# Kernel tuning notes

Measured on AMD Instinct MI355X. Metric: run time of the kernel, lower is better.

## Reference

```python
import jax, jax.numpy as jnp
import numpy as np

N_EMBD = 1024
HEAD_SIZE = 128
B, T = 8, 4096


def setup_inputs() -> dict:
    key = jax.random.key(0)
    ks = jax.random.split(key, 7)
    s = 1.0 / np.sqrt(N_EMBD)
    return {
        "x": jax.random.normal(ks[0], (B, T, N_EMBD), dtype=jnp.float32),
        "Wq": jax.random.uniform(ks[1], (N_EMBD, HEAD_SIZE), jnp.float32, -s, s),
        "bq": jax.random.uniform(ks[2], (HEAD_SIZE,), jnp.float32, -s, s),
        "Wk": jax.random.uniform(ks[3], (N_EMBD, HEAD_SIZE), jnp.float32, -s, s),
        "bk": jax.random.uniform(ks[4], (HEAD_SIZE,), jnp.float32, -s, s),
        "Wv": jax.random.uniform(ks[5], (N_EMBD, HEAD_SIZE), jnp.float32, -s, s),
        "bv": jax.random.uniform(ks[6], (HEAD_SIZE,), jnp.float32, -s, s),
    }


def reference(x, Wq, bq, Wk, bk, Wv, bv):
    # q,k,v: [B,T,H]
    q = x @ Wq + bq
    k = x @ Wk + bk
    v = x @ Wv + bv
    scale = HEAD_SIZE ** -0.5
    att = jnp.einsum("bth,bsh->bts", q, k) * scale  # [B,T,T]
    t = x.shape[1]
    causal = jnp.tril(jnp.ones((t, t), dtype=bool))
    att = jnp.where(causal, att, -jnp.inf)
    att = jax.nn.softmax(att, axis=-1)
    # dropout with p=0.0 is identity (eval-mode equivalent)
    out = jnp.einsum("bts,bsh->bth", att, v)  # [B,T,H]
    return out
```

## Files before the change

kernel.cpp:

```cpp
#include <hip/hip_runtime.h>
#include <hip/hip_bf16.h>
#include <stdint.h>

#define BATCH 8
#define SEQ   4096
#define EMB   1024
#define HD    128
#define NROWS 32768

typedef __attribute__((ext_vector_type(8))) short short8;
typedef __attribute__((ext_vector_type(4))) float f32x4;

__device__ inline unsigned short f2bf(float f) {
    union { float f; unsigned int u; } c; c.f = f;
    unsigned int u = c.u;
    unsigned int r = (u + 0x7fffu + ((u >> 16) & 1u)) >> 16;
    return (unsigned short)r;
}
__device__ inline float bf2f(unsigned short u) {
    union { unsigned int i; float f; } c; c.i = ((unsigned int)u) << 16; return c.f;
}
__device__ inline unsigned int pkbf(float a, float b) {
    __hip_bfloat162 h = __float22bfloat162_rn(make_float2(a, b));
    union { __hip_bfloat162 h; unsigned int u; } c; c.h = h; return c.u;
}

#define GLDS16(gp, lp) __builtin_amdgcn_global_load_lds( \
    (const __attribute__((address_space(1))) void*)(gp), \
    (__attribute__((address_space(3))) void*)(lp), 16, 0, 0)

__device__ inline void decomp(int it, int& b, int& qt, int& kv) {
    b = it / 2112;
    int r = it - b * 2112;
    int q = (int)((__builtin_sqrtf(2.0f * (float)r + 1.0f) - 1.0f) * 0.5f);
    while (2 * (q + 1) * (q + 2) <= r) ++q;
    while (2 * q * (q + 1) > r) --q;
    qt = q;
    kv = r - 2 * q * (q + 1);
}
__device__ inline int base1(int qt) {
    if (qt < 5)  return qt;
    if (qt < 11) return 5 + 2 * (qt - 5);
    if (qt < 16) return 17 + 3 * (qt - 11);
    if (qt < 22) return 32 + 4 * (qt - 16);
    if (qt < 27) return 56 + 5 * (qt - 22);
    return 81 + 6 * (qt - 27);
}

__global__ __launch_bounds__(256) void prep_kernel(
    const float* __restrict__ Wq, const float* __restrict__ bq,
    const float* __restrict__ Wk, const float* __restrict__ bk,
    const float* __restrict__ Wv, const float* __restrict__ bv,
    unsigned short* __restrict__ wt, float* __restrict__ biasc)
{
    const int n = blockIdx.x;
    const int sel = n >> 7, h = n & 127;
    const float* W = (sel == 0) ? Wq : (sel == 1) ? Wk : Wv;
    const int tid = threadIdx.x;
    const int k0 = tid * 4;
    union { unsigned short us[4]; uint2 v; } pk;
#pragma unroll
    for (int u = 0; u < 4; ++u) pk.us[u] = f2bf(W[(size_t)(k0 + u) * HD + h]);
    *(uint2*)&wt[(size_t)n * EMB + k0] = pk.v;
    if (tid == 0) {
        const float* bp = (sel == 0) ? bq : (sel == 1) ? bk : bv;
        biasc[n] = bp[h];
    }
}

__global__ __launch_bounds__(768, 3) void gemm_qkv(
    const float* __restrict__ x, const unsigned short* __restrict__ wt,
    const float* __restrict__ biasc,
    unsigned short* __restrict__ q, unsigned short* __restrict__ kOut,
    unsigned short* __restrict__ vt)
{
    const int m0  = blockIdx.x * 128;
    const int tid = threadIdx.x;
    const int wave = tid >> 6, lane = tid & 63;
    const int quad = lane >> 4, l15 = lane & 15;
    const int wm = (wave >= 6) ? 1 : 0;
    const int wn = wave - wm * 6;

    __shared__ __align__(16) unsigned short As[2][128][40];
    __shared__ __align__(16) unsigned short Bs[2][12288];

    f32x4 acc[4][4];
#pragma unroll
    for (int i = 0; i < 4; ++i)
#pragma unroll
        for (int j = 0; j < 4; ++j) acc[i][j] = (f32x4){0.f, 0.f, 0.f, 0.f};

    const int aactive = (tid < 512);
    const int arow = tid >> 3, akc = (tid & 7) * 4;
    float4 aR0, aR1;

#define LOAD_A(kt)                                                          \
    if (aactive) {                                                          \
        aR0 = *(const float4*)(x + (size_t)(m0 + arow) * EMB + (kt) * 32 + akc);        \
        aR1 = *(const float4*)(x + (size_t)(m0 + arow + 64) * EMB + (kt) * 32 + akc);   \
    }
#define WRITE_A(buf)                                                        \
    if (aactive) {                                                          \
        union { unsigned short us[4]; uint2 v; } p0, p1;                    \
        p0.us[0] = f2bf(aR0.x); p0.us[1] = f2bf(aR0.y);                     \
        p0.us[2] = f2bf(aR0.z); p0.us[3] = f2bf(aR0.w);                     \
        *(uint2*)&As[buf][arow][akc] = p0.v;                                \
        p1.us[0] = f2bf(aR1.x); p1.us[1] = f2bf(aR1.y);                     \
        p1.us[2] = f2bf(aR1.z); p1.us[3] = f2bf(aR1.w);                     \
        *(uint2*)&As[buf][arow + 64][akc] = p1.v;                           \
    }
#define STAGE_B(kt, buf)                                                    \
    {                                                                       \
        _Pragma("unroll")                                                   \
        for (int g = 0; g < 2; ++g) {                                       \
            int s0 = (g * 12 + wave) * 64;                                  \
            int s  = s0 + lane;                                             \
            int n  = s >> 2, c = (s & 3) ^ (n & 3);                         \
            GLDS16(wt + (size_t)n * EMB + (kt) * 32 + c * 8,                \
                   &Bs[buf][s0 * 8]);                                       \
        }                                                                   \
    }

    LOAD_A(0); STAGE_B(0, 0); WRITE_A(0);
    int cur = 0;

    for (int kt = 0; kt < 32; ++kt) {
        __syncthreads();
        if (kt < 31) { LOAD_A(kt + 1); STAGE_B(kt + 1, cur ^ 1); }
        short8 af[4], bw[4];
#pragma unroll
        for (int mj = 0; mj < 4; ++mj)
            af[mj] = *(const short8*)&As[cur][wm * 64 + mj * 16 + l15][quad * 8];
#pragma unroll
        for (int ni = 0; ni < 4; ++ni) {
            int n = wn * 64 + ni * 16 + l15;
            bw[ni] = *(const short8*)&Bs[cur][n * 32 + ((quad ^ (n & 3)) << 3)];
        }
#pragma unroll
        for (int ni = 0; ni < 4; ++ni)
#pragma unroll
            for (int mj = 0; mj < 4; ++mj)
                acc[ni][mj] = __builtin_amdgcn_mfma_f32_16x16x32_bf16(
                    bw[ni], af[mj], acc[ni][mj], 0, 0, 0);
        if (kt < 31) WRITE_A(cur ^ 1);
        cur ^= 1;
    }

    const float qscale = 0.08838834764831845f * 1.4426950408889634f;
    const int bb = m0 >> 12;
    const int t0 = m0 & 4095;
    const int mrow0 = m0 + wm * 64;
    const int tl0   = t0 + wm * 64;
#pragma unroll
    for (int ni = 0; ni < 4; ++ni) {
        int colbase = wn * 64 + ni * 16;
        int sel = colbase >> 7;
        int c0 = colbase + quad * 4;
        float4 bv4 = *(const float4*)&biasc[c0];
#pragma unroll
        for (int mj = 0; mj < 4; ++mj) {
            int m = mrow0 + mj * 16 + l15;
            if (sel == 0) {
                union { unsigned short us[4]; uint2 v; } pk;
#pragma unroll
                for (int j = 0; j < 4; ++j)
                    pk.us[j] = f2bf((acc[ni][mj][j] + ((const float*)&bv4)[j]) * qscale);
                *(uint2*)&q[(size_t)m * HD + (c0 & 127)] = pk.v;
            } else if (sel == 1) {
                union { unsigned short us[4]; uint2 v; } pk;
#pragma unroll
                for (int j = 0; j < 4; ++j)
                    pk.us[j] = f2bf(acc[ni][mj][j] + ((const float*)&bv4)[j]);
                *(uint2*)&kOut[(size_t)m * HD + (c0 & 127)] = pk.v;
            } else {
#pragma unroll
                for (int j = 0; j < 4; ++j) {
                    int h = (c0 & 127) + j;
                    vt[((size_t)(bb * 128 + h)) * SEQ + tl0 + mj * 16 + l15] =
                        f2bf(acc[ni][mj][j] + ((const float*)&bv4)[j]);
                }
            }
        }
    }
#undef LOAD_A
#undef WRITE_A
#undef STAGE_B
}

__global__ __launch_bounds__(256, 3) void attn_kernel(
    const unsigned short* __restrict__ q, const unsigned short* __restrict__ k,
    const unsigned short* __restrict__ vt, float* __restrict__ out,
    float* __restrict__ Oseg, float2* __restrict__ ml)
{
    const int rank  = blockIdx.x;
    const int chunk = (rank & 7) * 96 + (rank >> 3);
    const int start = chunk * 22;
    const int iend  = start + 22;

    const int tid  = threadIdx.x;
    const int wave = tid >> 6, lane = tid & 63;
    const int quad = lane >> 4, l15 = lane & 15;

    __shared__ __align__(16) unsigned short Ks[2][4096];
    __shared__ __align__(16) unsigned short Vs[2][4096];

    const int bpa0 = (l15 + 16 * ((2 * quad) & 3)) * 4;
    const int bpa1 = (l15 + 16 * ((2 * quad + 1) & 3)) * 4;

#define STAGE_KV(b_, kv_, buf_)                                              \
    {                                                                        \
        const size_t kb0 = (size_t)(b_) * SEQ + (kv_) * 32;                  \
        const size_t vb0 = (size_t)(b_) * HD * SEQ + (kv_) * 32;             \
        _Pragma("unroll")                                                    \
        for (int g = 0; g < 2; ++g) {                                        \
            int s0 = (g * 4 + wave) * 64;                                    \
            int s  = s0 + lane;                                              \
            int key = s >> 4, c = (s & 15) ^ (key & 15);                     \
            GLDS16(k + (kb0 + key) * HD + c * 8, &Ks[buf_][s0 * 8]);         \
        }                                                                    \
        _Pragma("unroll")                                                    \
        for (int g = 0; g < 2; ++g) {                                        \
            int s0 = (g * 4 + wave) * 64;                                    \
            int s  = s0 + lane;                                              \
            int h = s >> 2, c = (s & 3) ^ ((h >> 2) & 3);                    \
            GLDS16(vt + vb0 + (size_t)h * SEQ + c * 8, &Vs[buf_][s0 * 8]);   \
        }                                                                    \
    }

    int b, qt, kv;
    decomp(start, b, qt, kv);

    short8 qf[2][4];
    f32x4  o[2][8];
    float  m_r[2], l_r[2];
    int    qrow0 = 0;

#define CTX_INIT(b_, q_)                                                     \
    {                                                                        \
        qrow0 = (q_) * 128 + wave * 32;                                      \
        const size_t qoff = (size_t)(b_) * SEQ + qrow0;                      \
        _Pragma("unroll")                                                    \
        for (int mi = 0; mi < 2; ++mi)                                       \
            _Pragma("unroll")                                                \
            for (int kh = 0; kh < 4; ++kh)                                   \
                qf[mi][kh] = *(const short8*)(q + (qoff + mi * 16 + l15) * HD + kh * 32 + quad * 8); \
        _Pragma("unroll")                                                    \
        for (int mi = 0; mi < 2; ++mi) {                                     \
            _Pragma("unroll")                                                \
            for (int hi = 0; hi < 8; ++hi) o[mi][hi] = (f32x4){0.f, 0.f, 0.f, 0.f}; \
            m_r[mi] = -1e30f; l_r[mi] = 0.f;                                 \
        }                                                                    \
    }

#define CTX_FLUSH()                                                          \
    {                                                                        \
        const int I0 = b * 2112 + 2 * qt * (qt + 1);                         \
        const int j  = chunk - I0 / 22;                                      \
        const int rr = wave * 32;                                            \
        float* obase;                                                        \
        if (j == 0) obase = out + ((size_t)b * SEQ + qrow0) * HD;            \
        else obase = Oseg + ((size_t)(b * 112 + base1(qt) + j - 1) * 128 + rr) * HD; \
        const size_t mlb = ((size_t)(b * 32 + qt) * 7 + j) * 128 + rr;       \
        _Pragma("unroll")                                                    \
        for (int mi = 0; mi < 2; ++mi) {                                     \
            if (quad == 0) ml[mlb + mi * 16 + l15] = make_float2(m_r[mi], l_r[mi]); \
            _Pragma("unroll")                                                \
            for (int hi = 0; hi < 8; ++hi)                                   \
                *(f32x4*)&obase[(size_t)(mi * 16 + l15) * HD + hi * 16 + quad * 4] = o[mi][hi]; \
        }                                                                    \
    }

#define SMAX(sarr, mi_, pk_)                                                 \
    {                                                                        \
        float mx = fmaxf(fmaxf(fmaxf(sarr[0][0], sarr[0][1]),               \
                               fmaxf(sarr[0][2], sarr[0][3])),              \
                         fmaxf(fmaxf(sarr[1][0], sarr[1][1]),               \
                               fmaxf(sarr[1][2], sarr[1][3])));             \
        mx = fmaxf(mx, __shfl_xor(mx, 16));                                  \
        mx = fmaxf(mx, __shfl_xor(mx, 32));                                  \
        if (!__all(mx - m_r[mi_] <= 8.0f)) {                                 \
            float mnew = fmaxf(m_r[mi_], mx);                                \
            float alpha = __builtin_amdgcn_exp2f(m_r[mi_] - mnew);           \
            m_r[mi_] = mnew;                                                 \
            l_r[mi_] *= alpha;                                               \
            _Pragma("unroll")                                                \
            for (int hi = 0; hi < 8; ++hi) o[mi_][hi] *= alpha;              \
        }                                                                    \
        const float mcur = m_r[mi_];                                         \
        float rs = 0.f;                                                      \
        _Pragma("unroll")                                                    \
        for (int ni = 0; ni < 2; ++ni) {                                     \
            float p0 = __builtin_amdgcn_exp2f(sarr[ni][0] - mcur);           \
            float p1 = __builtin_amdgcn_exp2f(sarr[ni][1] - mcur);           \
            float p2 = __builtin_amdgcn_exp2f(sarr[ni][2] - mcur);           \
            float p3 = __builtin_amdgcn_exp2f(sarr[ni][3] - mcur);           \
            rs += (p0 + p1) + (p2 + p3);                                     \
            pk_[ni][0] = pkbf(p0, p1);                                       \
            pk_[ni][1] = pkbf(p2, p3);                                       \
        }                                                                    \
        rs += __shfl_xor(rs, 16);                                            \
        rs += __shfl_xor(rs, 32);                                            \
        l_r[mi_] += rs;                                                      \
    }

#define BPERM(pk_, pT_)                                                      \
    {                                                                        \
        union { unsigned int u[4]; short8 s8; } pt;                          \
        unsigned int a0 = (unsigned)__builtin_amdgcn_ds_bpermute(bpa0, (int)pk_[0][0]); \
        unsigned int b0 = (unsigned)__builtin_amdgcn_ds_bpermute(bpa0, (int)pk_[1][0]); \
        pt.u[0] = (quad < 2) ? a0 : b0;                                      \
        unsigned int a1 = (unsigned)__builtin_amdgcn_ds_bpermute(bpa0, (int)pk_[0][1]); \
        unsigned int b1 = (unsigned)__builtin_amdgcn_ds_bpermute(bpa0, (int)pk_[1][1]); \
        pt.u[1] = (quad < 2) ? a1 : b1;                                      \
        unsigned int a2 = (unsigned)__builtin_amdgcn_ds_bpermute(bpa1, (int)pk_[0][0]); \
        unsigned int b2 = (unsigned)__builtin_amdgcn_ds_bpermute(bpa1, (int)pk_[1][0]); \
        pt.u[2] = (quad < 2) ? a2 : b2;                                      \
        unsigned int a3 = (unsigned)__builtin_amdgcn_ds_bpermute(bpa1, (int)pk_[0][1]); \
        unsigned int b3 = (unsigned)__builtin_amdgcn_ds_bpermute(bpa1, (int)pk_[1][1]); \
        pt.u[3] = (quad < 2) ? a3 : b3;                                      \
        pT_ = pt.s8;                                                         \
    }

    STAGE_KV(b, kv, 0);
    CTX_INIT(b, qt);
    int cur = 0;

    for (int it = start; it < iend; ++it) {
        const bool more = (it + 1 < iend);
        int b2 = b, qt2 = qt, kv2 = kv + 1;
        const bool ctxend = (kv2 == 4 * qt + 4);
        if (ctxend) { kv2 = 0; ++qt2; if (qt2 == 32) { qt2 = 0; ++b2; } }

        __syncthreads();
        if (more) STAGE_KV(b2, kv2, cur ^ 1);

        const int key0 = kv * 32;
        if (key0 <= qrow0 + 31) {
            f32x4 s0[2], s1[2];
#pragma unroll
            for (int ni = 0; ni < 2; ++ni) { s0[ni] = (f32x4){0.f,0.f,0.f,0.f}; s1[ni] = (f32x4){0.f,0.f,0.f,0.f}; }
            __builtin_amdgcn_s_setprio(1);
#pragma unroll
            for (int kh = 0; kh < 4; ++kh) {
#pragma unroll
                for (int ni = 0; ni < 2; ++ni) {
                    short8 kf = *(const short8*)&Ks[cur][(ni * 16 + l15) * 128 + (((kh * 4 + quad) ^ l15) << 3)];
                    s0[ni] = __builtin_amdgcn_mfma_f32_16x16x32_bf16(kf, qf[0][kh], s0[ni], 0, 0, 0);
                    s1[ni] = __builtin_amdgcn_mfma_f32_16x16x32_bf16(kf, qf[1][kh], s1[ni], 0, 0, 0);
                }
            }
            __builtin_amdgcn_s_setprio(0);
            if (key0 + 31 > qrow0) {
#pragma unroll
                for (int ni = 0; ni < 2; ++ni)
#pragma unroll
                    for (int j = 0; j < 4; ++j) {
                        int key = key0 + ni * 16 + quad * 4 + j;
                        if (key > qrow0 + l15)      s0[ni][j] = -1e30f;
                        if (key > qrow0 + 16 + l15) s1[ni][j] = -1e30f;
                    }
            }
            unsigned int pk0[2][2], pk1[2][2];
            short8 pT0, pT1;
            SMAX(s0, 0, pk0)
            BPERM(pk0, pT0)
            SMAX(s1, 1, pk1)
            BPERM(pk1, pT1)
            __builtin_amdgcn_s_setprio(1);
#pragma unroll
            for (int hi = 0; hi < 8; ++hi) {
                short8 vf = *(const short8*)&Vs[cur][(hi * 16 + l15) * 32 + ((quad ^ (l15 >> 2)) << 3)];
                o[0][hi] = __builtin_amdgcn_mfma_f32_16x16x32_bf16(vf, pT0, o[0][hi], 0, 0, 0);
                o[1][hi] = __builtin_amdgcn_mfma_f32_16x16x32_bf16(vf, pT1, o[1][hi], 0, 0, 0);
            }
            __builtin_amdgcn_s_setprio(0);
        }

        if (ctxend || !more) {
            CTX_FLUSH();
            if (more && ctxend) CTX_INIT(b2, qt2);
        }
        b = b2; qt = qt2; kv = kv2;
        cur ^= 1;
    }
#undef STAGE_KV
#undef CTX_INIT
#undef CTX_FLUSH
#undef SMAX
#undef BPERM
}

__global__ __launch_bounds__(256) void merge_kernel(
    float* __restrict__ out, const float* __restrict__ Oseg,
    const float2* __restrict__ ml)
{
    int idx = blockIdx.x * 256 + threadIdx.x;
    int row = idx >> 5;
    int hc  = (idx & 31) << 2;
    int b = row >> 12, t = row & 4095, qt = t >> 7, rr = t & 127;
    int I0   = b * 2112 + 2 * qt * (qt + 1);
    int n    = 4 * (qt + 1);
    int nseg = (I0 + n - 1) / 22 - I0 / 22 + 1;

    const float2* mlp = ml + ((size_t)(b * 32 + qt) * 7) * 128 + rr;
    float2 s0 = mlp[0];
    float M = s0.x;
    for (int j = 1; j < nseg; ++j) M = fmaxf(M, mlp[(size_t)j * 128].x);

    float w0 = __builtin_amdgcn_exp2f(s0.x - M);
    float L  = w0 * s0.y;
    f32x4 a = *(const f32x4*)&out[(size_t)row * HD + hc];
    a = a * w0;
    for (int j = 1; j < nseg; ++j) {
        float2 mj = mlp[(size_t)j * 128];
        float w = __builtin_amdgcn_exp2f(mj.x - M);
        L += w * mj.y;
        const float* sp = Oseg + ((size_t)(b * 112 + base1(qt) + j - 1) * 128 + rr) * HD + hc;
        f32x4 sv = *(const f32x4*)sp;
        a = a + sv * w;
    }
    float inv = 1.0f / L;
    *(f32x4*)&out[(size_t)row * HD + hc] = a * inv;
}

extern "C" void kernel_launch(void* const* d_in, const int* in_sizes, int n_in,
                              void* d_out, int out_size, void* d_ws, size_t ws_size,
                              hipStream_t stream) {
    const float* x  = (const float*)d_in[0];
    const float* Wq = (const float*)d_in[1];
    const float* bq = (const float*)d_in[2];
    const float* Wk = (const float*)d_in[3];
    const float* bk = (const float*)d_in[4];
    const float* Wv = (const float*)d_in[5];
    const float* bv = (const float*)d_in[6];
    float* out = (float*)d_out;

    unsigned short* wt    = (unsigned short*)d_ws;
    float*          biasc = (float*)((char*)d_ws + 786432);
    unsigned short* qb    = (unsigned short*)((char*)d_ws + 787968);
    unsigned short* kb    = qb  + (size_t)NROWS * HD;
    unsigned short* vtb   = kb  + (size_t)NROWS * HD;
    float*          Oseg  = (float*)((char*)d_ws + 787968 + 3ull * NROWS * HD * 2);
    float2*         mlseg = (float2*)((char*)Oseg + 896ull * 128 * HD * 4);

    prep_kernel<<<dim3(384), 256, 0, stream>>>(Wq, bq, Wk, bk, Wv, bv, wt, biasc);
    gemm_qkv<<<dim3(256), 768, 0, stream>>>(x, wt, biasc, qb, kb, vtb);
    attn_kernel<<<dim3(768), 256, 0, stream>>>(qb, kb, vtb, out, Oseg, mlseg);
    merge_kernel<<<dim3(NROWS * 32 / 256), 256, 0, stream>>>(out, Oseg, mlseg);
}
```

Measured before the change: 308.8 us.

## Triple-buffer K/V staging with vmcnt-based waits in attention kernel

Measured after the change: 315.0 us. 1.02x slower.

```diff
diff --git a/kernel.cpp b/kernel.cpp
--- a/kernel.cpp
+++ b/kernel.cpp
@@ -195,14 +195,14 @@
     const int rank  = blockIdx.x;
     const int chunk = (rank & 7) * 96 + (rank >> 3);
     const int start = chunk * 22;
-    const int iend  = start + 22;
+    const int ITEMS = 22;
 
     const int tid  = threadIdx.x;
     const int wave = tid >> 6, lane = tid & 63;
     const int quad = lane >> 4, l15 = lane & 15;
 
-    __shared__ __align__(16) unsigned short Ks[2][4096];
-    __shared__ __align__(16) unsigned short Vs[2][4096];
+    __shared__ __align__(16) unsigned short Ks[3][4096];
+    __shared__ __align__(16) unsigned short Vs[3][4096];
 
     const int bpa0 = (l15 + 16 * ((2 * quad) & 3)) * 4;
     const int bpa1 = (l15 + 16 * ((2 * quad + 1) & 3)) * 4;
@@ -226,6 +226,12 @@
             GLDS16(vt + vb0 + (size_t)h * SEQ + c * 8, &Vs[buf_][s0 * 8]);   \
         }                                                                    \
     }
+
+#define ADV(b_, q_, k_)                                                      \
+    { if (++k_ == 4 * q_ + 4) { k_ = 0; if (++q_ == 32) { q_ = 0; ++b_; } } }
+
+#define PIPE_WAIT4() { asm volatile("s_waitcnt vmcnt(4)\n\ts_barrier" ::: "memory"); __builtin_amdgcn_sched_barrier(0); }
+#define PIPE_WAIT0() { asm volatile("s_waitcnt vmcnt(0)\n\ts_barrier" ::: "memory"); __builtin_amdgcn_sched_barrier(0); }
 
     int b, qt, kv;
     decomp(start, b, qt, kv);
@@ -266,7 +272,8 @@
             if (quad == 0) ml[mlb + mi * 16 + l15] = make_float2(m_r[mi], l_r[mi]); \
             _Pragma("unroll")                                                \
             for (int hi = 0; hi < 8; ++hi)                                   \
-                *(f32x4*)&obase[(size_t)(mi * 16 + l15) * HD + hi * 16 + quad * 4] = o[mi][hi]; \
+                __builtin_nontemporal_store(o[mi][hi],                        \
+                    (f32x4*)&obase[(size_t)(mi * 16 + l15) * HD + hi * 16 + quad * 4]); \
         }                                                                    \
     }
 
@@ -321,18 +328,22 @@
         pT_ = pt.s8;                                                         \
     }
 
+    int b1 = b, q1 = qt, k1 = kv; ADV(b1, q1, k1);
+    int bs = b1, qs = q1, ks = k1; ADV(bs, qs, ks);
     STAGE_KV(b, kv, 0);
+    STAGE_KV(b1, k1, 1);
+    PIPE_WAIT4();
     CTX_INIT(b, qt);
+
     int cur = 0;
-
-    for (int it = start; it < iend; ++it) {
-        const bool more = (it + 1 < iend);
-        int b2 = b, qt2 = qt, kv2 = kv + 1;
-        const bool ctxend = (kv2 == 4 * qt + 4);
-        if (ctxend) { kv2 = 0; ++qt2; if (qt2 == 32) { qt2 = 0; ++b2; } }
-
-        __syncthreads();
-        if (more) STAGE_KV(b2, kv2, cur ^ 1);
+    for (int j = 0; j < ITEMS; ++j) {
+        const bool more  = (j + 1 < ITEMS);
+        const bool more2 = (j + 2 < ITEMS);
+        if (more2) {
+            int bufn = cur + 2; if (bufn >= 3) bufn -= 3;
+            STAGE_KV(bs, ks, bufn);
+            ADV(bs, qs, ks);
+        }
 
         const int key0 = kv * 32;
         if (key0 <= qrow0 + 31) {
@@ -354,10 +365,10 @@
 #pragma unroll
                 for (int ni = 0; ni < 2; ++ni)
 #pragma unroll
-                    for (int j = 0; j < 4; ++j) {
-                        int key = key0 + ni * 16 + quad * 4 + j;
-                        if (key > qrow0 + l15)      s0[ni][j] = -1e30f;
-                        if (key > qrow0 + 16 + l15) s1[ni][j] = -1e30f;
+                    for (int jj = 0; jj < 4; ++jj) {
+                        int key = key0 + ni * 16 + quad * 4 + jj;
+                        if (key > qrow0 + l15)      s0[ni][jj] = -1e30f;
+                        if (key > qrow0 + 16 + l15) s1[ni][jj] = -1e30f;
                     }
             }
             unsigned int pk0[2][2], pk1[2][2];
@@ -376,14 +387,22 @@
             __builtin_amdgcn_s_setprio(0);
         }
 
+        const bool ctxend = (kv == 4 * qt + 3);
+        int b2 = b, q2 = qt, k2 = kv; ADV(b2, q2, k2);
+
+        if (more) { if (more2) PIPE_WAIT4() else PIPE_WAIT0() }
+
         if (ctxend || !more) {
             CTX_FLUSH();
-            if (more && ctxend) CTX_INIT(b2, qt2);
+            if (more && ctxend) CTX_INIT(b2, q2);
         }
-        b = b2; qt = qt2; kv = kv2;
-        cur ^= 1;
+        b = b2; qt = q2; kv = k2;
+        if (++cur == 3) cur = 0;
     }
 #undef STAGE_KV
+#undef ADV
+#undef PIPE_WAIT4
+#undef PIPE_WAIT0
 #undef CTX_INIT
 #undef CTX_FLUSH
 #undef SMAX
```
